# Performance work log

Hardware: AMD Instinct MI355X
Metric: run time of the kernel (lower is better)

Reference implementation:

```python
import jax, jax.numpy as jnp
import numpy as np

IGNORE_INDEX = -100
BETA = 0.1

def setup_inputs() -> dict:
    key = jax.random.key(0)
    k1, k2, k3, k4, k5, k6 = jax.random.split(key, 6)
    B, T, H, V = 4, 512, 2048, 32000
    x = jax.random.normal(k1, (B, T, H), dtype=jnp.float32)
    ref_x = jax.random.normal(k2, (B, T, H), dtype=jnp.float32)
    y = jax.random.randint(k3, (B, T), 0, V, dtype=jnp.int64)
    # mask a prefix of each sequence with ignore_index to exercise masking
    y = y.at[:, :10].set(IGNORE_INDEX)
    preference_labels = jax.random.randint(k4, (B,), 0, 2) == 1
    scale = 1.0 / np.sqrt(H)
    W = jax.random.normal(k5, (V, H), dtype=jnp.float32) * scale      # policy lm_head weight
    ref_W = jax.random.normal(k6, (V, H), dtype=jnp.float32) * scale  # reference lm_head weight
    return {"x": x, "ref_x": ref_x, "y": y, "preference_labels": preference_labels,
            "W": W, "ref_W": ref_W}


def _avg_target_logps(inp, w, y):
    # inp: (B, T, H), w: (V, H), y: (B, T) -> per-sequence average log-prob (B,)
    logits = jnp.einsum("bth,vh->btv", inp, w)
    logps = jax.nn.log_softmax(logits.astype(jnp.float32), axis=-1)
    mask = y != IGNORE_INDEX
    labels = jnp.where(mask, y, 0)
    tok_logps = jnp.take_along_axis(logps, labels[..., None], axis=-1)[..., 0]
    return (tok_logps * mask).sum(-1) / mask.sum(-1)


def reference(x, ref_x, y, preference_labels, W, ref_W):
    policy_logps = _avg_target_logps(x, W, y)                              # (B,)
    ref_logps = jax.lax.stop_gradient(_avg_target_logps(ref_x, ref_W, y))  # ref model under no_grad
    logratios = policy_logps - ref_logps
    multiplier = jnp.where(preference_labels, 1.0, -1.0)
    # KTO loss with KL term = 0 (policy_KL_logps / ref_KL_logps are None)
    losses = 1.0 - jax.nn.sigmoid(BETA * logratios * multiplier)
    return losses.sum() / y.shape[0]
```

## Files before the change

kernel.cpp:

```cpp
#include <hip/hip_runtime.h>
#include <math.h>

#define BATCH 4
#define TSEQ 512
#define MTOK 2048
#define HDIM 2048
#define VOCAB 32000
#define NCHUNK 500
#define IGNORE_INDEX (-100)
#define BETA 0.1f

#define WSCALE 16.0f
#define SCALE_ONE  0x7F7F7F7F
#define SCALE_W    0x7B7B7B7B

#define CVT_PER_BLOCK 8192
#define WCVT_BLK (VOCAB * HDIM / 4 / CVT_PER_BLOCK)
#define XCVT_BLK (MTOK * HDIM / 4 / CVT_PER_BLOCK)

typedef __attribute__((ext_vector_type(4))) float floatx4;
typedef __attribute__((ext_vector_type(4))) int   intx4;
typedef __attribute__((ext_vector_type(8))) int   intx8;

__device__ __forceinline__ void async_copy16b(const unsigned char* g, unsigned char* l) {
    __builtin_amdgcn_global_load_lds(
        (const __attribute__((address_space(1))) void*)g,
        (__attribute__((address_space(3))) void*)l, 16, 0, 0);
}

__device__ __forceinline__ void cvtq_run(const float* __restrict__ src,
                                         unsigned int* __restrict__ dst,
                                         int relblk, float scale) {
    size_t base = (size_t)relblk * CVT_PER_BLOCK + threadIdx.x;
    const floatx4* s4 = (const floatx4*)src;
#pragma unroll
    for (int k = 0; k < 32; ++k) {
        floatx4 a = s4[base + k * 256];
        int lo  = __builtin_amdgcn_cvt_pk_fp8_f32(a[0] * scale, a[1] * scale, 0,  false);
        int all = __builtin_amdgcn_cvt_pk_fp8_f32(a[2] * scale, a[3] * scale, lo, true);
        dst[base + k * 256] = (unsigned int)all;
    }
}

__global__ __launch_bounds__(256) void cvtq_all_kernel(
        const float* __restrict__ s0, const float* __restrict__ s1,
        const float* __restrict__ s2, const float* __restrict__ s3,
        unsigned int* __restrict__ d0, unsigned int* __restrict__ d1,
        unsigned int* __restrict__ d2, unsigned int* __restrict__ d3) {
    int b = blockIdx.x;
    if (b < WCVT_BLK)                     cvtq_run(s0, d0, b, WSCALE);
    else if (b < 2 * WCVT_BLK)            cvtq_run(s1, d1, b - WCVT_BLK, WSCALE);
    else if (b < 2 * WCVT_BLK + XCVT_BLK) cvtq_run(s2, d2, b - 2 * WCVT_BLK, 1.0f);
    else                                  cvtq_run(s3, d3, b - 2 * WCVT_BLK - XCVT_BLK, 1.0f);
}

__global__ __launch_bounds__(256) void cvtq_one_kernel(
        const float* __restrict__ src, unsigned int* __restrict__ dst, float scale) {
    cvtq_run(src, dst, blockIdx.x, scale);
}

#define BKF 128
#define BM  256
#define BN  256
#define VPANELS 125
#define GRIDY   128

__device__ __forceinline__ intx8 frag_ld(const unsigned char* base, int row, int q) {
    const int p0 = (2 * q) ^ (row & 7);
    const intx4 lo = *(const intx4*)(base + row * BKF + p0 * 16);
    const intx4 hi = *(const intx4*)(base + row * BKF + (p0 ^ 1) * 16);
    intx8 v;
    v[0] = lo[0]; v[1] = lo[1]; v[2] = lo[2]; v[3] = lo[3];
    v[4] = hi[0]; v[5] = hi[1]; v[6] = hi[2]; v[7] = hi[3];
    return v;
}

#define MFMA8(ACC_I, ACC_J, AF, BF)                                           \
    _Pragma("unroll")                                                         \
    for (int i = 0; i < 4; ++i) {                                             \
        _Pragma("unroll")                                                     \
        for (int j = 0; j < 2; ++j)                                           \
            acc[(ACC_I) + i][(ACC_J) + j] =                                   \
                __builtin_amdgcn_mfma_scale_f32_16x16x128_f8f6f4(             \
                    AF[i], BF[j], acc[(ACC_I) + i][(ACC_J) + j],              \
                    0, 0, 0, SCALE_ONE, 0, SCALE_W);                          \
    }

#define STG(gp, ls, hh, kk) do {                                                          \
    async_copy16b((gp) + (size_t)(hh) * 128 * HDIM + (kk),            (ls) + (hh) * 16384 + e0); \
    async_copy16b((gp) + (size_t)(hh) * 128 * HDIM + 64 * HDIM + (kk),(ls) + (hh) * 16384 + 8192 + e0); \
} while (0)

__global__ __launch_bounds__(512, 2) void gemm_lse_fp8_kernel(
        const unsigned char* __restrict__ Xq0,
        const unsigned char* __restrict__ Xq1,
        const unsigned char* __restrict__ Wq0,
        const unsigned char* __restrict__ Wq1,
        const int* __restrict__ y,
        float* __restrict__ pmax,
        float* __restrict__ psum,
        float* __restrict__ tlog,
        int slot_base)
{
    const int lin = blockIdx.x + (int)(gridDim.x) * blockIdx.y;
    const int xcd = lin & 7;
    const int t   = lin >> 3;
    const int bx  = (xcd & 1) * 4 + (t & 3);
    const int by  = (xcd >> 1) * 32 + (t >> 2);
    if (by >= VPANELS) return;

    __shared__ __align__(16) unsigned char sAB[2][2][BM * BKF];

    const int slot = slot_base + blockIdx.z;
    const unsigned char* __restrict__ Xq = slot ? Xq1 : Xq0;
    const unsigned char* __restrict__ Wq = slot ? Wq1 : Wq0;

    const int tid  = threadIdx.x;
    const int m0   = bx * BM;
    const int v0   = by * BN;
    const int w    = tid >> 6;
    const int lane = tid & 63;
    const int wm   = w >> 2;
    const int wn   = w & 3;
    const int c    = lane & 15;
    const int q    = lane >> 4;

    const int e0    = tid * 16;
    const int srow  = e0 >> 7;
    const int colsw = (((e0 >> 4) & 7) ^ (srow & 7)) * 16;
    const unsigned char* aP = Xq + (size_t)(m0 + srow) * HDIM + colsw;
    const unsigned char* bP = Wq + (size_t)(v0 + srow) * HDIM + colsw;

    unsigned char* const L0A = &sAB[0][0][0];
    unsigned char* const L0B = &sAB[0][1][0];
    unsigned char* const L1B = &sAB[1][1][0];

    STG(bP, L0B, 0, 0);
    STG(bP, L0B, 1, 0);
    STG(aP, L0A, 0, 0);
    STG(aP, L0A, 1, 0);
    STG(bP, L1B, 0, BKF);
    STG(bP, L1B, 1, BKF);

    floatx4 acc[8][4] = {};
    const int arow = wm * 128 + c;
    const int brow = wn * 64 + c;

    asm volatile("s_waitcnt vmcnt(4)" ::: "memory");
    __builtin_amdgcn_s_barrier();

    for (int u = 0; u < HDIM / BKF; ++u) {
        unsigned char* const A  = &sAB[u & 1][0][0];
        unsigned char* const B  = &sAB[u & 1][1][0];
        unsigned char* const NA = &sAB[(u + 1) & 1][0][0];
        const int kk1 = ((u + 1) & 15) * BKF;
        const int kk2 = ((u + 2) & 15) * BKF;

        intx8 afl[4], afh[4], bfa[2], bfb[2];

#pragma unroll
        for (int i = 0; i < 4; ++i) afl[i] = frag_ld(A, arow + i * 16, q);
#pragma unroll
        for (int j = 0; j < 2; ++j) bfa[j] = frag_ld(B, brow + j * 16, q);
#pragma unroll
        for (int j = 0; j < 2; ++j) bfb[j] = frag_ld(B, brow + 32 + j * 16, q);
        __builtin_amdgcn_s_barrier();
        asm volatile("s_waitcnt lgkmcnt(0)" ::: "memory");
        __builtin_amdgcn_sched_barrier(0);
        __builtin_amdgcn_s_setprio(1);
        MFMA8(0, 0, afl, bfa);
        MFMA8(0, 2, afl, bfb);
        __builtin_amdgcn_s_setprio(0);
        __builtin_amdgcn_s_barrier();

        STG(aP, NA, 0, kk1);
        STG(aP, NA, 1, kk1);
        STG(bP, B, 0, kk2);
        STG(bP, B, 1, kk2);
#pragma unroll
        for (int i = 0; i < 4; ++i) afh[i] = frag_ld(A, arow + 64 + i * 16, q);
        __builtin_amdgcn_s_barrier();
        asm volatile("s_waitcnt lgkmcnt(0)" ::: "memory");
        __builtin_amdgcn_sched_barrier(0);
        __builtin_amdgcn_s_setprio(1);
        MFMA8(4, 0, afh, bfa);
        MFMA8(4, 2, afh, bfb);
        __builtin_amdgcn_s_setprio(0);
        asm volatile("s_waitcnt vmcnt(4)" ::: "memory");
        __builtin_amdgcn_s_barrier();
    }

    const int chunk = by * 4 + wn;
#pragma unroll
    for (int i = 0; i < 8; ++i) {
        float mx[4], sm[4];
#pragma unroll
        for (int r = 0; r < 4; ++r) {
            float m4 = acc[i][0][r];
            m4 = fmaxf(m4, acc[i][1][r]);
            m4 = fmaxf(m4, acc[i][2][r]);
            m4 = fmaxf(m4, acc[i][3][r]);
            mx[r] = m4;
        }
#pragma unroll
        for (int d = 1; d < 16; d <<= 1)
#pragma unroll
            for (int r = 0; r < 4; ++r)
                mx[r] = fmaxf(mx[r], __shfl_xor(mx[r], d, 64));
#pragma unroll
        for (int r = 0; r < 4; ++r) {
            float s = 0.f;
#pragma unroll
            for (int j = 0; j < 4; ++j) s += expf(acc[i][j][r] - mx[r]);
            sm[r] = s;
        }
#pragma unroll
        for (int d = 1; d < 16; d <<= 1)
#pragma unroll
            for (int r = 0; r < 4; ++r)
                sm[r] += __shfl_xor(sm[r], d, 64);

        const int tokenBase = m0 + wm * 128 + i * 16 + q * 4;
        if (c == 0) {
#pragma unroll
            for (int r = 0; r < 4; ++r) {
                pmax[(size_t)(slot * MTOK + tokenBase + r) * NCHUNK + chunk] = mx[r];
                psum[(size_t)(slot * MTOK + tokenBase + r) * NCHUNK + chunk] = sm[r];
            }
        }
#pragma unroll
        for (int r = 0; r < 4; ++r) {
            int lab = y[tokenBase + r];
            int rel = lab - (v0 + wn * 64);
            if (rel >= 0 && rel < 64 && (rel & 15) == c) {
#pragma unroll
                for (int j = 0; j < 4; ++j)
                    if ((rel >> 4) == j)
                        tlog[(size_t)slot * MTOK + tokenBase + r] = acc[i][j][r];
            }
        }
    }
}

__global__ __launch_bounds__(256) void finalize_kernel(
        const int* __restrict__ y,
        const float* __restrict__ pmax,
        const float* __restrict__ psum,
        const float* __restrict__ tlog,
        float* __restrict__ tokll, int slot_base) {
    const int wv    = threadIdx.x >> 6;
    const int lane  = threadIdx.x & 63;
    const int token = blockIdx.x * 4 + wv;
    const int slot  = slot_base + blockIdx.y;

    const float* pm = &pmax[(size_t)(slot * MTOK + token) * NCHUNK];
    const float* ps = &psum[(size_t)(slot * MTOK + token) * NCHUNK];
    float m = -3.4e38f, s = 0.f;
    for (int c2 = lane; c2 < NCHUNK; c2 += 64) {
        float cm = pm[c2];
        float cs = ps[c2];
        if (cm > m) { s = s * expf(m - cm) + cs; m = cm; }
        else        { s += cs * expf(cm - m); }
    }
#pragma unroll
    for (int d = 1; d < 64; d <<= 1) {
        float om = __shfl_xor(m, d, 64);
        float os = __shfl_xor(s, d, 64);
        if (om > m) { s = s * expf(m - om) + os; m = om; }
        else        { s += os * expf(om - m); }
    }
    if (lane == 0) {
        int lab = y[token];
        float lse = m + logf(s);
        tokll[(size_t)slot * MTOK + token] =
            (lab == IGNORE_INDEX) ? 0.f : (tlog[(size_t)slot * MTOK + token] - lse);
    }
}

__global__ __launch_bounds__(256) void tail_kernel(
        const int* __restrict__ y,
        const float* __restrict__ tokll,
        const int* __restrict__ pref,
        float* __restrict__ out) {
    __shared__ float rs[256];
    __shared__ float rc[256];
    __shared__ float seqavg[8];
    const int tid = threadIdx.x;
    for (int sb = 0; sb < 8; ++sb) {
        const int slot = sb >> 2;
        const int b    = sb & 3;
        float lsum = 0.f, lcnt = 0.f;
        for (int t = tid; t < TSEQ; t += 256) {
            int token = b * TSEQ + t;
            lsum += tokll[(size_t)slot * MTOK + token];
            lcnt += (y[token] != IGNORE_INDEX) ? 1.f : 0.f;
        }
        rs[tid] = lsum; rc[tid] = lcnt;
        __syncthreads();
        for (int s2 = 128; s2 > 0; s2 >>= 1) {
            if (tid < s2) { rs[tid] += rs[tid + s2]; rc[tid] += rc[tid + s2]; }
            __syncthreads();
        }
        if (tid == 0) seqavg[sb] = rs[0] / rc[0];
        __syncthreads();
    }
    if (tid == 0) {
        float acc = 0.f;
        for (int b = 0; b < BATCH; ++b) {
            float lr   = seqavg[b] - seqavg[BATCH + b];
            float mult = pref[b] ? 1.f : -1.f;
            float z    = BETA * lr * mult;
            float sig  = 1.f / (1.f + expf(-z));
            acc += 1.f - sig;
        }
        out[0] = acc * (1.f / (float)BATCH);
    }
}

extern "C" void kernel_launch(void* const* d_in, const int* in_sizes, int n_in,
                              void* d_out, int out_size, void* d_ws, size_t ws_size,
                              hipStream_t stream) {
    const float* x      = (const float*)d_in[0];
    const float* ref_x  = (const float*)d_in[1];
    const int*   y      = (const int*)d_in[2];
    const int*   pref   = (const int*)d_in[3];
    const float* W      = (const float*)d_in[4];
    const float* ref_W  = (const float*)d_in[5];
    float* out = (float*)d_out;
    char*  ws  = (char*)d_ws;

    const size_t WQSZ = (size_t)VOCAB * HDIM;
    const size_t XQSZ = (size_t)MTOK * HDIM;
    const size_t PSZ  = (size_t)2 * MTOK * NCHUNK * 4;

    const size_t need_dual = 2*WQSZ + 2*XQSZ + 2*PSZ + (size_t)4*MTOK*4 + 4096;

    if (ws_size >= need_dual) {
        unsigned char* wq0 = (unsigned char*)(ws);
        unsigned char* wq1 = (unsigned char*)(ws + WQSZ);
        unsigned char* xq0 = (unsigned char*)(ws + 2*WQSZ);
        unsigned char* xq1 = (unsigned char*)(ws + 2*WQSZ + XQSZ);
        float* pmax  = (float*)(ws + 2*WQSZ + 2*XQSZ);
        float* psum  = (float*)(ws + 2*WQSZ + 2*XQSZ + PSZ);
        float* tlog  = (float*)(ws + 2*WQSZ + 2*XQSZ + 2*PSZ);
        float* tokll = (float*)(ws + 2*WQSZ + 2*XQSZ + 2*PSZ + (size_t)2*MTOK*4);

        cvtq_all_kernel<<<2*WCVT_BLK + 2*XCVT_BLK, 256, 0, stream>>>(
            W, ref_W, x, ref_x,
            (unsigned int*)wq0, (unsigned int*)wq1,
            (unsigned int*)xq0, (unsigned int*)xq1);
        gemm_lse_fp8_kernel<<<dim3(MTOK/BM, GRIDY, 2), 512, 0, stream>>>(
            xq0, xq1, wq0, wq1, y, pmax, psum, tlog, 0);
        finalize_kernel<<<dim3(MTOK/4, 2), 256, 0, stream>>>(
            y, pmax, psum, tlog, tokll, 0);
        tail_kernel<<<1, 256, 0, stream>>>(y, tokll, pref, out);
    } else {
        unsigned char* wq = (unsigned char*)(ws);
        unsigned char* xq = (unsigned char*)(ws + WQSZ);
        float* pmax  = (float*)(ws + WQSZ + XQSZ);
        float* psum  = (float*)(ws + WQSZ + XQSZ + PSZ);
        float* tlog  = (float*)(ws + WQSZ + XQSZ + 2*PSZ);
        float* tokll = (float*)(ws + WQSZ + XQSZ + 2*PSZ + (size_t)2*MTOK*4);

        for (int model = 0; model < 2; ++model) {
            const float* xin = model ? ref_x : x;
            const float* win = model ? ref_W : W;
            cvtq_one_kernel<<<WCVT_BLK, 256, 0, stream>>>(win, (unsigned int*)wq, WSCALE);
            cvtq_one_kernel<<<XCVT_BLK, 256, 0, stream>>>(xin, (unsigned int*)xq, 1.0f);
            gemm_lse_fp8_kernel<<<dim3(MTOK/BM, GRIDY, 1), 512, 0, stream>>>(
                xq, xq, wq, wq, y, pmax, psum, tlog, model);
            finalize_kernel<<<dim3(MTOK/4, 1), 256, 0, stream>>>(
                y, pmax, psum, tlog, tokll, model);
        }
        tail_kernel<<<1, 256, 0, stream>>>(y, tokll, pref, out);
    }
}
```

Before: 930.2 us.

## Shrink GEMM tiles to 128x128 with a simple single-buffered K loop

Replaces the 256x256-tile, 512-thread, double-buffered MFMA pipeline with 128x128 tiles on 256-thread blocks. The K loop becomes a plain load, sync, MFMA, sync sequence, and the grid gets a new XCD-aware block mapping. The goal is more blocks, better occupancy and simpler scheduling. The cost is lost load/compute overlap, more global traffic from reduced tile reuse, and twice as many barriers per K step.

```diff
diff --git a/kernel.cpp b/kernel.cpp
--- a/kernel.cpp
+++ b/kernel.cpp
@@ -60,10 +60,10 @@
 }
 
 #define BKF 128
-#define BM  256
-#define BN  256
-#define VPANELS 125
-#define GRIDY   128
+#define BM  128
+#define BN  128
+#define VPANELS 250
+#define GRIDY   512
 
 __device__ __forceinline__ intx8 frag_ld(const unsigned char* base, int row, int q) {
     const int p0 = (2 * q) ^ (row & 7);
@@ -75,23 +75,7 @@
     return v;
 }
 
-#define MFMA8(ACC_I, ACC_J, AF, BF)                                           \
-    _Pragma("unroll")                                                         \
-    for (int i = 0; i < 4; ++i) {                                             \
-        _Pragma("unroll")                                                     \
-        for (int j = 0; j < 2; ++j)                                           \
-            acc[(ACC_I) + i][(ACC_J) + j] =                                   \
-                __builtin_amdgcn_mfma_scale_f32_16x16x128_f8f6f4(             \
-                    AF[i], BF[j], acc[(ACC_I) + i][(ACC_J) + j],              \
-                    0, 0, 0, SCALE_ONE, 0, SCALE_W);                          \
-    }
-
-#define STG(gp, ls, hh, kk) do {                                                          \
-    async_copy16b((gp) + (size_t)(hh) * 128 * HDIM + (kk),            (ls) + (hh) * 16384 + e0); \
-    async_copy16b((gp) + (size_t)(hh) * 128 * HDIM + 64 * HDIM + (kk),(ls) + (hh) * 16384 + 8192 + e0); \
-} while (0)
-
-__global__ __launch_bounds__(512, 2) void gemm_lse_fp8_kernel(
+__global__ __launch_bounds__(256, 2) void gemm_lse_fp8_kernel(
         const unsigned char* __restrict__ Xq0,
         const unsigned char* __restrict__ Xq1,
         const unsigned char* __restrict__ Wq0,
@@ -102,14 +86,14 @@
         float* __restrict__ tlog,
         int slot_base)
 {
-    const int lin = blockIdx.x + (int)(gridDim.x) * blockIdx.y;
-    const int xcd = lin & 7;
-    const int t   = lin >> 3;
-    const int bx  = (xcd & 1) * 4 + (t & 3);
-    const int by  = (xcd >> 1) * 32 + (t >> 2);
+    const int xcd = blockIdx.x;
+    const int t   = blockIdx.y;
+    const int bx  = (t & 7) + 8 * (t >> 8);
+    const int by  = xcd * 32 + ((t >> 3) & 31);
     if (by >= VPANELS) return;
 
-    __shared__ __align__(16) unsigned char sAB[2][2][BM * BKF];
+    __shared__ __align__(16) unsigned char sA[BM * BKF];
+    __shared__ __align__(16) unsigned char sB[BN * BKF];
 
     const int slot = slot_base + blockIdx.z;
     const unsigned char* __restrict__ Xq = slot ? Xq1 : Xq0;
@@ -120,8 +104,8 @@
     const int v0   = by * BN;
     const int w    = tid >> 6;
     const int lane = tid & 63;
-    const int wm   = w >> 2;
-    const int wn   = w & 3;
+    const int wm   = w >> 1;
+    const int wn   = w & 1;
     const int c    = lane & 15;
     const int q    = lane >> 4;
 
@@ -131,68 +115,38 @@
     const unsigned char* aP = Xq + (size_t)(m0 + srow) * HDIM + colsw;
     const unsigned char* bP = Wq + (size_t)(v0 + srow) * HDIM + colsw;
 
-    unsigned char* const L0A = &sAB[0][0][0];
-    unsigned char* const L0B = &sAB[0][1][0];
-    unsigned char* const L1B = &sAB[1][1][0];
-
-    STG(bP, L0B, 0, 0);
-    STG(bP, L0B, 1, 0);
-    STG(aP, L0A, 0, 0);
-    STG(aP, L0A, 1, 0);
-    STG(bP, L1B, 0, BKF);
-    STG(bP, L1B, 1, BKF);
-
-    floatx4 acc[8][4] = {};
-    const int arow = wm * 128 + c;
+    floatx4 acc[4][4] = {};
+    const int arow = wm * 64 + c;
     const int brow = wn * 64 + c;
 
-    asm volatile("s_waitcnt vmcnt(4)" ::: "memory");
-    __builtin_amdgcn_s_barrier();
-
-    for (int u = 0; u < HDIM / BKF; ++u) {
-        unsigned char* const A  = &sAB[u & 1][0][0];
-        unsigned char* const B  = &sAB[u & 1][1][0];
-        unsigned char* const NA = &sAB[(u + 1) & 1][0][0];
-        const int kk1 = ((u + 1) & 15) * BKF;
-        const int kk2 = ((u + 2) & 15) * BKF;
-
-        intx8 afl[4], afh[4], bfa[2], bfb[2];
-
-#pragma unroll
-        for (int i = 0; i < 4; ++i) afl[i] = frag_ld(A, arow + i * 16, q);
-#pragma unroll
-        for (int j = 0; j < 2; ++j) bfa[j] = frag_ld(B, brow + j * 16, q);
-#pragma unroll
-        for (int j = 0; j < 2; ++j) bfb[j] = frag_ld(B, brow + 32 + j * 16, q);
-        __builtin_amdgcn_s_barrier();
-        asm volatile("s_waitcnt lgkmcnt(0)" ::: "memory");
-        __builtin_amdgcn_sched_barrier(0);
-        __builtin_amdgcn_s_setprio(1);
-        MFMA8(0, 0, afl, bfa);
-        MFMA8(0, 2, afl, bfb);
-        __builtin_amdgcn_s_setprio(0);
-        __builtin_amdgcn_s_barrier();
-
-        STG(aP, NA, 0, kk1);
-        STG(aP, NA, 1, kk1);
-        STG(bP, B, 0, kk2);
-        STG(bP, B, 1, kk2);
-#pragma unroll
-        for (int i = 0; i < 4; ++i) afh[i] = frag_ld(A, arow + 64 + i * 16, q);
-        __builtin_amdgcn_s_barrier();
-        asm volatile("s_waitcnt lgkmcnt(0)" ::: "memory");
-        __builtin_amdgcn_sched_barrier(0);
-        __builtin_amdgcn_s_setprio(1);
-        MFMA8(4, 0, afh, bfa);
-        MFMA8(4, 2, afh, bfb);
-        __builtin_amdgcn_s_setprio(0);
-        asm volatile("s_waitcnt vmcnt(4)" ::: "memory");
-        __builtin_amdgcn_s_barrier();
-    }
-
-    const int chunk = by * 4 + wn;
-#pragma unroll
-    for (int i = 0; i < 8; ++i) {
+    for (int kt = 0; kt < HDIM / BKF; ++kt) {
+        const int kk = kt * BKF;
+#pragma unroll
+        for (int r = 0; r < 4; ++r)
+            async_copy16b(aP + (size_t)r * 32 * HDIM + kk, &sA[r * 4096 + e0]);
+#pragma unroll
+        for (int r = 0; r < 4; ++r)
+            async_copy16b(bP + (size_t)r * 32 * HDIM + kk, &sB[r * 4096 + e0]);
+        __syncthreads();
+
+        intx8 af[4], bf[4];
+#pragma unroll
+        for (int i = 0; i < 4; ++i) af[i] = frag_ld(sA, arow + i * 16, q);
+#pragma unroll
+        for (int j = 0; j < 4; ++j) bf[j] = frag_ld(sB, brow + j * 16, q);
+#pragma unroll
+        for (int i = 0; i < 4; ++i)
+#pragma unroll
+            for (int j = 0; j < 4; ++j)
+                acc[i][j] = __builtin_amdgcn_mfma_scale_f32_16x16x128_f8f6f4(
+                    af[i], bf[j], acc[i][j],
+                    0, 0, 0, SCALE_ONE, 0, SCALE_W);
+        __syncthreads();
+    }
+
+    const int chunk = by * 2 + wn;
+#pragma unroll
+    for (int i = 0; i < 4; ++i) {
         float mx[4], sm[4];
 #pragma unroll
         for (int r = 0; r < 4; ++r) {
@@ -220,7 +174,7 @@
             for (int r = 0; r < 4; ++r)
                 sm[r] += __shfl_xor(sm[r], d, 64);
 
-        const int tokenBase = m0 + wm * 128 + i * 16 + q * 4;
+        const int tokenBase = m0 + wm * 64 + i * 16 + q * 4;
         if (c == 0) {
 #pragma unroll
             for (int r = 0; r < 4; ++r) {
@@ -349,7 +303,7 @@
             W, ref_W, x, ref_x,
             (unsigned int*)wq0, (unsigned int*)wq1,
             (unsigned int*)xq0, (unsigned int*)xq1);
-        gemm_lse_fp8_kernel<<<dim3(MTOK/BM, GRIDY, 2), 512, 0, stream>>>(
+        gemm_lse_fp8_kernel<<<dim3(8, GRIDY, 2), 256, 0, stream>>>(
             xq0, xq1, wq0, wq1, y, pmax, psum, tlog, 0);
         finalize_kernel<<<dim3(MTOK/4, 2), 256, 0, stream>>>(
             y, pmax, psum, tlog, tokll, 0);
@@ -367,7 +321,7 @@
             const float* win = model ? ref_W : W;
             cvtq_one_kernel<<<WCVT_BLK, 256, 0, stream>>>(win, (unsigned int*)wq, WSCALE);
             cvtq_one_kernel<<<XCVT_BLK, 256, 0, stream>>>(xin, (unsigned int*)xq, 1.0f);
-            gemm_lse_fp8_kernel<<<dim3(MTOK/BM, GRIDY, 1), 512, 0, stream>>>(
+            gemm_lse_fp8_kernel<<<dim3(8, GRIDY, 1), 256, 0, stream>>>(
                 xq, xq, wq, wq, y, pmax, psum, tlog, model);
             finalize_kernel<<<dim3(MTOK/4, 1), 256, 0, stream>>>(
                 y, pmax, psum, tlog, tokll, model);
```

After: 2.867 ms. 208% more time.
